# Optimization experiments

Measured on AMD Instinct MI355X. Metric: run time of the kernel, lower is better.

Reference implementation:

```python
import jax, jax.numpy as jnp
import numpy as np
import math

N_EMBD = 1024
N_HEAD = 16
B, T = 2, 2048


def new_gelu(x):
    # GPT-2 tanh-approx GELU (matches torch module exactly)
    return 0.5 * x * (1.0 + jnp.tanh(jnp.sqrt(2.0 / jnp.pi) * (x + 0.044715 * x ** 3)))


def layer_norm(x, w, b, eps=1e-5):
    mu = jnp.mean(x, axis=-1, keepdims=True)
    var = jnp.var(x, axis=-1, keepdims=True)
    return (x - mu) * jax.lax.rsqrt(var + eps) * w + b


def setup_inputs() -> dict:
    key = jax.random.key(0)
    ks = jax.random.split(key, 8)
    C = N_EMBD
    s = 0.02
    return {
        "x": jax.random.normal(ks[0], (B, T, C), dtype=jnp.float32),
        "ln1_w": jnp.ones((C,), jnp.float32),
        "ln1_b": jnp.zeros((C,), jnp.float32),
        "attn_w": s * jax.random.normal(ks[1], (C, 3 * C), jnp.float32),
        "attn_b": jnp.zeros((3 * C,), jnp.float32),
        "attn_proj_w": s * jax.random.normal(ks[2], (C, C), jnp.float32),
        "attn_proj_b": jnp.zeros((C,), jnp.float32),
        "ln2_w": jnp.ones((C,), jnp.float32),
        "ln2_b": jnp.zeros((C,), jnp.float32),
        "fc_w": s * jax.random.normal(ks[3], (C, 4 * C), jnp.float32),
        "fc_b": jnp.zeros((4 * C,), jnp.float32),
        "mlp_proj_w": s * jax.random.normal(ks[4], (4 * C, C), jnp.float32),
        "mlp_proj_b": jnp.zeros((C,), jnp.float32),
    }


def block_forward(x, ln1_w, ln1_b, attn_w, attn_b, attn_proj_w, attn_proj_b,
                  ln2_w, ln2_b, fc_w, fc_b, mlp_proj_w, mlp_proj_b):
    Bm, Tm, C = x.shape
    H = N_HEAD
    D = C // H
    # --- self attention (pre-LN) ---
    h = layer_norm(x, ln1_w, ln1_b)
    qkv = h @ attn_w + attn_b  # [B,T,3C]
    q, k, v = jnp.split(qkv, 3, axis=-1)
    q = q.reshape(Bm, Tm, H, D).transpose(0, 2, 1, 3)  # [B,H,T,D]
    k = k.reshape(Bm, Tm, H, D).transpose(0, 2, 1, 3)
    v = v.reshape(Bm, Tm, H, D).transpose(0, 2, 1, 3)
    att = jnp.einsum('bhqd,bhkd->bhqk', q, k) * (1.0 / math.sqrt(D))
    att = jax.nn.softmax(att, axis=-1)  # NOTE: no causal mask in source
    y = jnp.einsum('bhqk,bhkd->bhqd', att, v)
    y = y.transpose(0, 2, 1, 3).reshape(Bm, Tm, C)
    x = x + (y @ attn_proj_w + attn_proj_b)
    # --- MLP ---
    h = layer_norm(x, ln2_w, ln2_b)
    h = new_gelu(h @ fc_w + fc_b)
    x = x + (h @ mlp_proj_w + mlp_proj_b)
    return x


def reference(x, ln1_w, ln1_b, attn_w, attn_b, attn_proj_w, attn_proj_b,
              ln2_w, ln2_b, fc_w, fc_b, mlp_proj_w, mlp_proj_b):
    return block_forward(x, ln1_w, ln1_b, attn_w, attn_b, attn_proj_w, attn_proj_b,
                         ln2_w, ln2_b, fc_w, fc_b, mlp_proj_w, mlp_proj_b)
```

## Files before the change

kernel.cpp:

```cpp
#include <hip/hip_runtime.h>

typedef __attribute__((ext_vector_type(4)))  float  f32x4;
typedef __attribute__((ext_vector_type(16))) float  f32x16;
typedef __attribute__((ext_vector_type(8)))  short  s16x8;
typedef __attribute__((ext_vector_type(4)))  short  s16x4;
typedef __attribute__((ext_vector_type(4)))  unsigned u32x4;
typedef __attribute__((ext_vector_type(2)))  unsigned u32x2;
typedef __attribute__((ext_vector_type(2)))  int    i32x2;

__device__ __forceinline__ short f2bf(float f) {
    unsigned u = __builtin_bit_cast(unsigned, f);
    u += 0x7fff + ((u >> 16) & 1);
    return (short)(u >> 16);
}

__device__ __forceinline__ void load_lds16(const void* g, void* l) {
    __builtin_amdgcn_global_load_lds(
        (const __attribute__((address_space(1))) unsigned int*)g,
        (__attribute__((address_space(3))) unsigned int*)l, 16, 0, 0);
}

__global__ __launch_bounds__(256) void transpose_cast(const float* __restrict__ W,
                                                      short* __restrict__ Wt,
                                                      int K, int N) {
    __shared__ float t[32][33];
    int n0 = blockIdx.x * 32, k0 = blockIdx.y * 32;
    int tx = threadIdx.x & 31, ty = threadIdx.x >> 5;
#pragma unroll
    for (int i = 0; i < 4; i++)
        t[ty + 8 * i][tx] = W[(size_t)(k0 + ty + 8 * i) * N + n0 + tx];
    __syncthreads();
#pragma unroll
    for (int i = 0; i < 4; i++)
        Wt[(size_t)(n0 + ty + 8 * i) * K + k0 + tx] = f2bf(t[tx][ty + 8 * i]);
}

__global__ __launch_bounds__(256) void vtrans_kernel(const short* __restrict__ qkv,
                                                     short* __restrict__ Vtg) {
    const int T = 2048, C3 = 3072;
    __shared__ short tl[32][33];
    int bh = blockIdx.y >> 1;
    int b = bh >> 4, h = bh & 15;
    int dh = (blockIdx.y & 1) * 32;
    int t0 = blockIdx.x * 32;
    int tx = threadIdx.x & 31, ty = threadIdx.x >> 5;
    const short* src = qkv + (size_t)b * T * C3 + 2048 + h * 64 + dh;
#pragma unroll
    for (int i = 0; i < 4; i++)
        tl[ty + 8 * i][tx] = src[(size_t)(t0 + ty + 8 * i) * C3 + tx];
    __syncthreads();
#pragma unroll
    for (int i = 0; i < 4; i++)
        Vtg[((size_t)bh * 64 + dh + ty + 8 * i) * T + t0 + tx] = tl[tx][ty + 8 * i];
}

__global__ __launch_bounds__(256) void ln_kernel(const float* __restrict__ x,
                                                 const float* __restrict__ w,
                                                 const float* __restrict__ b,
                                                 short* __restrict__ out) {
    int row = blockIdx.x;
    int tid = threadIdx.x;
    const float4 v = ((const float4*)(x + (size_t)row * 1024))[tid];
    float s  = v.x + v.y + v.z + v.w;
    float ss = v.x * v.x + v.y * v.y + v.z * v.z + v.w * v.w;
#pragma unroll
    for (int o = 32; o > 0; o >>= 1) {
        s  += __shfl_down(s, o);
        ss += __shfl_down(ss, o);
    }
    __shared__ float rs[4], rq[4];
    int wave = tid >> 6, lane = tid & 63;
    if (lane == 0) { rs[wave] = s; rq[wave] = ss; }
    __syncthreads();
    float tot = rs[0] + rs[1] + rs[2] + rs[3];
    float tq  = rq[0] + rq[1] + rq[2] + rq[3];
    float mu   = tot * (1.f / 1024.f);
    float var  = tq * (1.f / 1024.f) - mu * mu;
    float rstd = rsqrtf(var + 1e-5f);
    const float4 wv = ((const float4*)w)[tid];
    const float4 bv = ((const float4*)b)[tid];
    s16x4 o;
    o[0] = f2bf((v.x - mu) * rstd * wv.x + bv.x);
    o[1] = f2bf((v.y - mu) * rstd * wv.y + bv.y);
    o[2] = f2bf((v.z - mu) * rstd * wv.z + bv.z);
    o[3] = f2bf((v.w - mu) * rstd * wv.w + bv.w);
    ((s16x4*)(out + (size_t)row * 1024))[tid] = o;
}

template <typename OUT_T, bool GELU, bool RES, bool SCALE_Q>
__global__ __launch_bounds__(256) void gemm_bt(const short* __restrict__ A,
                                               const short* __restrict__ Bt,
                                               const float* __restrict__ bias,
                                               const float* __restrict__ res,
                                               OUT_T* __restrict__ C,
                                               int M, int N, int K) {
    __shared__ __align__(16) short As[128 * 32];
    __shared__ __align__(16) short Bs[128 * 32];
    int tid = threadIdx.x;
    int m0 = blockIdx.y * 128, n0 = blockIdx.x * 128;
    int wave = tid >> 6, lane = tid & 63;
    int wr = wave >> 1, wc = wave & 1;
    int g = lane >> 4, q = lane & 15;
    f32x4 acc[4][4] = {};
    const short* Ab = A + (size_t)m0 * K;
    const short* Bb = Bt + (size_t)n0 * K;
    int srow = tid >> 2;
    int scol = (tid & 3) * 8;
    for (int k0 = 0; k0 < K; k0 += 32) {
        __syncthreads();
        load_lds16(Ab + (size_t)srow * K + k0 + scol, As + tid * 8);
        load_lds16(Ab + (size_t)(srow + 64) * K + k0 + scol, As + 2048 + tid * 8);
        load_lds16(Bb + (size_t)srow * K + k0 + scol, Bs + tid * 8);
        load_lds16(Bb + (size_t)(srow + 64) * K + k0 + scol, Bs + 2048 + tid * 8);
        __syncthreads();
        s16x8 a[4], bf[4];
#pragma unroll
        for (int mi = 0; mi < 4; mi++)
            a[mi] = *(const s16x8*)(As + (wr * 64 + mi * 16 + q) * 32 + g * 8);
#pragma unroll
        for (int ni = 0; ni < 4; ni++)
            bf[ni] = *(const s16x8*)(Bs + (wc * 64 + ni * 16 + q) * 32 + g * 8);
#pragma unroll
        for (int mi = 0; mi < 4; mi++)
#pragma unroll
            for (int ni = 0; ni < 4; ni++)
                acc[mi][ni] = __builtin_amdgcn_mfma_f32_16x16x32_bf16(a[mi], bf[ni], acc[mi][ni], 0, 0, 0);
    }
#pragma unroll
    for (int mi = 0; mi < 4; mi++) {
#pragma unroll
        for (int ni = 0; ni < 4; ni++) {
            int row = m0 + wr * 64 + mi * 16 + g * 4;
            int col = n0 + wc * 64 + ni * 16 + q;
            float bb = bias[col];
#pragma unroll
            for (int r = 0; r < 4; r++) {
                float v = acc[mi][ni][r] + bb;
                if (RES) v += res[(size_t)(row + r) * N + col];
                if (GELU) {
                    float aa = 0.7978845608028654f * (v + 0.044715f * v * v * v);
                    float th = 1.f - 2.f / (__expf(2.f * aa) + 1.f);
                    v = 0.5f * v * (1.f + th);
                }
                if (SCALE_Q && col < 1024) v *= 0.18033688011112042f;
                if constexpr (sizeof(OUT_T) == 2)
                    C[(size_t)(row + r) * N + col] = f2bf(v);
                else
                    C[(size_t)(row + r) * N + col] = v;
            }
        }
    }
}

__global__ __launch_bounds__(256) void gemm_bt_sk(const short* __restrict__ A,
                                                  const short* __restrict__ Bt,
                                                  float* __restrict__ part,
                                                  int M, int N, int K, int Klen) {
    __shared__ __align__(16) short As[128 * 32];
    __shared__ __align__(16) short Bs[128 * 32];
    int tid = threadIdx.x;
    int m0 = blockIdx.y * 128, n0 = blockIdx.x * 128;
    int kz = blockIdx.z;
    int wave = tid >> 6, lane = tid & 63;
    int wr = wave >> 1, wc = wave & 1;
    int g = lane >> 4, q = lane & 15;
    f32x4 acc[4][4] = {};
    const short* Ab = A + (size_t)m0 * K;
    const short* Bb = Bt + (size_t)n0 * K;
    int srow = tid >> 2;
    int scol = (tid & 3) * 8;
    int kend = kz * Klen + Klen;
    for (int k0 = kz * Klen; k0 < kend; k0 += 32) {
        __syncthreads();
        load_lds16(Ab + (size_t)srow * K + k0 + scol, As + tid * 8);
        load_lds16(Ab + (size_t)(srow + 64) * K + k0 + scol, As + 2048 + tid * 8);
        load_lds16(Bb + (size_t)srow * K + k0 + scol, Bs + tid * 8);
        load_lds16(Bb + (size_t)(srow + 64) * K + k0 + scol, Bs + 2048 + tid * 8);
        __syncthreads();
        s16x8 a[4], bf[4];
#pragma unroll
        for (int mi = 0; mi < 4; mi++)
            a[mi] = *(const s16x8*)(As + (wr * 64 + mi * 16 + q) * 32 + g * 8);
#pragma unroll
        for (int ni = 0; ni < 4; ni++)
            bf[ni] = *(const s16x8*)(Bs + (wc * 64 + ni * 16 + q) * 32 + g * 8);
#pragma unroll
        for (int mi = 0; mi < 4; mi++)
#pragma unroll
            for (int ni = 0; ni < 4; ni++)
                acc[mi][ni] = __builtin_amdgcn_mfma_f32_16x16x32_bf16(a[mi], bf[ni], acc[mi][ni], 0, 0, 0);
    }
    float* pb = part + (size_t)kz * M * N;
#pragma unroll
    for (int mi = 0; mi < 4; mi++) {
#pragma unroll
        for (int ni = 0; ni < 4; ni++) {
            int row = m0 + wr * 64 + mi * 16 + g * 4;
            int col = n0 + wc * 64 + ni * 16 + q;
#pragma unroll
            for (int r = 0; r < 4; r++)
                pb[(size_t)(row + r) * N + col] = acc[mi][ni][r];
        }
    }
}

template <int SK>
__global__ __launch_bounds__(256) void reduce_sk(const float* __restrict__ part,
                                                 const float* __restrict__ bias,
                                                 const float* __restrict__ res,
                                                 float* __restrict__ out,
                                                 int MN, int N) {
    int tot = MN >> 2;
    int nb4 = (N >> 2) - 1;
    for (int i = blockIdx.x * 256 + threadIdx.x; i < tot; i += gridDim.x * 256) {
        float4 s = ((const float4*)part)[i];
#pragma unroll
        for (int k = 1; k < SK; k++) {
            float4 p = ((const float4*)(part + (size_t)k * MN))[i];
            s.x += p.x; s.y += p.y; s.z += p.z; s.w += p.w;
        }
        float4 bv = ((const float4*)bias)[i & nb4];
        float4 rv = ((const float4*)res)[i];
        float4 o;
        o.x = s.x + bv.x + rv.x;
        o.y = s.y + bv.y + rv.y;
        o.z = s.z + bv.z + rv.z;
        o.w = s.w + bv.w + rv.w;
        ((float4*)out)[i] = o;
    }
}

__global__ __launch_bounds__(256) void attn_kernel(const short* __restrict__ qkv,
                                                   const short* __restrict__ Vtg,
                                                   short* __restrict__ y) {
    const int T = 2048, C3 = 3072;
    int wg = blockIdx.x;
    int mapped = (wg & 7) * 64 + (wg >> 3);
    int bh = mapped >> 4, qt = mapped & 15;
    int b = bh >> 4, h = bh & 15;
    int tid = threadIdx.x, lane = tid & 63, wave = tid >> 6;
    int ql = lane & 31, hi = lane >> 5;
    const short* base = qkv + (size_t)b * T * C3;

    int qrow = qt * 128 + wave * 32 + ql;
    const short* qp = base + (size_t)qrow * C3 + h * 64;
    s16x8 qf[4];
#pragma unroll
    for (int s = 0; s < 4; s++)
        qf[s] = *(const s16x8*)(qp + ((2 * s + hi) << 3));

    __shared__ __align__(16) short Ks[2][64 * 64];
    __shared__ __align__(16) short Vs[2][64 * 64];

    int srow = tid >> 3, sc8 = tid & 7;
    const short* ksrc = base + 1024 + h * 64 + (size_t)srow * C3 + ((sc8 ^ (srow & 7)) << 3);
    const short* vsrc = Vtg + ((size_t)bh * 64 + srow) * T + ((sc8 ^ (srow & 7)) << 3);

    auto stage = [&](int bi, int t) {
        const short* kp = ksrc + (size_t)(t * 64) * C3;
        load_lds16(kp, &Ks[bi][tid * 8]);
        load_lds16(kp + (size_t)32 * C3, &Ks[bi][tid * 8 + 2048]);
        const short* vp = vsrc + t * 64;
        load_lds16(vp, &Vs[bi][tid * 8]);
        load_lds16(vp + (size_t)32 * T, &Vs[bi][tid * 8 + 2048]);
    };

    float mst = -INFINITY, lst = 0.f;
    f32x16 accY0 = {}, accY1 = {};
    int swz = ql & 7;

    stage(0, 0);
    for (int t = 0; t < 32; ++t) {
        int cur = t & 1;
        __syncthreads();
        if (t < 31) stage(cur ^ 1, t + 1);
        f32x16 s0 = {}, s1 = {};
        const short* kb0 = &Ks[cur][ql * 64];
        const short* kb1 = &Ks[cur][(32 + ql) * 64];
        __builtin_amdgcn_s_setprio(1);
#pragma unroll
        for (int s = 0; s < 4; s++) {
            int c = ((2 * s + hi) ^ swz) << 3;
            s16x8 k0 = *(const s16x8*)(kb0 + c);
            s16x8 k1 = *(const s16x8*)(kb1 + c);
            s0 = __builtin_amdgcn_mfma_f32_32x32x16_bf16(k0, qf[s], s0, 0, 0, 0);
            s1 = __builtin_amdgcn_mfma_f32_32x32x16_bf16(k1, qf[s], s1, 0, 0, 0);
        }
        __builtin_amdgcn_s_setprio(0);
        float tm = fmaxf(s0[0], s0[1]);
#pragma unroll
        for (int r = 2; r < 16; r++) tm = fmaxf(tm, s0[r]);
#pragma unroll
        for (int r = 0; r < 16; r++) tm = fmaxf(tm, s1[r]);
        tm = fmaxf(tm, __shfl_xor(tm, 32));
        if (!__all(tm <= mst + 8.f)) {
            float mnew = fmaxf(mst, tm);
            float alpha = exp2f(mst - mnew);
            lst *= alpha;
#pragma unroll
            for (int r = 0; r < 16; r++) { accY0[r] *= alpha; accY1[r] *= alpha; }
            mst = mnew;
        }
        float ps = 0.f;
#pragma unroll
        for (int r = 0; r < 16; r++) { s0[r] = exp2f(s0[r] - mst); ps += s0[r]; }
#pragma unroll
        for (int r = 0; r < 16; r++) { s1[r] = exp2f(s1[r] - mst); ps += s1[r]; }
        ps += __shfl_xor(ps, 32);
        lst += ps;
        s16x8 pb[4];
#pragma unroll
        for (int s = 0; s < 4; s++) {
            int tt = (s & 1) * 8;
            unsigned lo0, lo1, hi0, hi1;
            if (s < 2) {
                asm("v_cvt_pk_bf16_f32 %0, %1, %2" : "=v"(lo0) : "v"(s0[tt + 0]), "v"(s0[tt + 1]));
                asm("v_cvt_pk_bf16_f32 %0, %1, %2" : "=v"(lo1) : "v"(s0[tt + 2]), "v"(s0[tt + 3]));
                asm("v_cvt_pk_bf16_f32 %0, %1, %2" : "=v"(hi0) : "v"(s0[tt + 4]), "v"(s0[tt + 5]));
                asm("v_cvt_pk_bf16_f32 %0, %1, %2" : "=v"(hi1) : "v"(s0[tt + 6]), "v"(s0[tt + 7]));
            } else {
                asm("v_cvt_pk_bf16_f32 %0, %1, %2" : "=v"(lo0) : "v"(s1[tt + 0]), "v"(s1[tt + 1]));
                asm("v_cvt_pk_bf16_f32 %0, %1, %2" : "=v"(lo1) : "v"(s1[tt + 2]), "v"(s1[tt + 3]));
                asm("v_cvt_pk_bf16_f32 %0, %1, %2" : "=v"(hi0) : "v"(s1[tt + 4]), "v"(s1[tt + 5]));
                asm("v_cvt_pk_bf16_f32 %0, %1, %2" : "=v"(hi1) : "v"(s1[tt + 6]), "v"(s1[tt + 7]));
            }
            i32x2 r0 = __builtin_amdgcn_permlane32_swap((int)hi0, (int)lo0, false, false);
            i32x2 r1 = __builtin_amdgcn_permlane32_swap((int)hi1, (int)lo1, false, false);
            u32x4 w;
            w[0] = (unsigned)r0[1]; w[1] = (unsigned)r1[1];
            w[2] = (unsigned)r0[0]; w[3] = (unsigned)r1[0];
            pb[s] = __builtin_bit_cast(s16x8, w);
        }
        const short* vb0 = &Vs[cur][ql * 64];
        const short* vb1 = &Vs[cur][(32 + ql) * 64];
        __builtin_amdgcn_s_setprio(1);
#pragma unroll
        for (int s = 0; s < 4; s++) {
            int c = ((2 * s + hi) ^ swz) << 3;
            s16x8 v0 = *(const s16x8*)(vb0 + c);
            s16x8 v1 = *(const s16x8*)(vb1 + c);
            accY0 = __builtin_amdgcn_mfma_f32_32x32x16_bf16(v0, pb[s], accY0, 0, 0, 0);
            accY1 = __builtin_amdgcn_mfma_f32_32x32x16_bf16(v1, pb[s], accY1, 0, 0, 0);
        }
        __builtin_amdgcn_s_setprio(0);
    }
    float linv = 1.f / lst;
    short* yrow = y + ((size_t)b * T + qrow) * 1024 + h * 64;
#pragma unroll
    for (int r = 0; r < 4; r++) {
        unsigned w0, w1, w2, w3;
        float a0 = accY0[4 * r] * linv, a1 = accY0[4 * r + 1] * linv;
        float a2 = accY0[4 * r + 2] * linv, a3 = accY0[4 * r + 3] * linv;
        float b0 = accY1[4 * r] * linv, b1 = accY1[4 * r + 1] * linv;
        float b2 = accY1[4 * r + 2] * linv, b3 = accY1[4 * r + 3] * linv;
        asm("v_cvt_pk_bf16_f32 %0, %1, %2" : "=v"(w0) : "v"(a0), "v"(a1));
        asm("v_cvt_pk_bf16_f32 %0, %1, %2" : "=v"(w1) : "v"(a2), "v"(a3));
        asm("v_cvt_pk_bf16_f32 %0, %1, %2" : "=v"(w2) : "v"(b0), "v"(b1));
        asm("v_cvt_pk_bf16_f32 %0, %1, %2" : "=v"(w3) : "v"(b2), "v"(b3));
        u32x2 p0; p0[0] = w0; p0[1] = w1;
        u32x2 p1; p1[0] = w2; p1[1] = w3;
        *(u32x2*)(yrow + 8 * r + 4 * hi)      = p0;
        *(u32x2*)(yrow + 32 + 8 * r + 4 * hi) = p1;
    }
}

extern "C" void kernel_launch(void* const* d_in, const int* in_sizes, int n_in,
                              void* d_out, int out_size, void* d_ws, size_t ws_size,
                              hipStream_t stream) {
    const float* x           = (const float*)d_in[0];
    const float* ln1_w       = (const float*)d_in[1];
    const float* ln1_b       = (const float*)d_in[2];
    const float* attn_w      = (const float*)d_in[3];
    const float* attn_b      = (const float*)d_in[4];
    const float* attn_proj_w = (const float*)d_in[5];
    const float* attn_proj_b = (const float*)d_in[6];
    const float* ln2_w       = (const float*)d_in[7];
    const float* ln2_b       = (const float*)d_in[8];
    const float* fc_w        = (const float*)d_in[9];
    const float* fc_b        = (const float*)d_in[10];
    const float* mlp_proj_w  = (const float*)d_in[11];
    const float* mlp_proj_b  = (const float*)d_in[12];

    const int M = 4096;

    size_t off = 0;
    char* wsb = (char*)d_ws;
    auto alloc = [&](size_t bytes) {
        void* p = wsb + off;
        off += (bytes + 255) & ~(size_t)255;
        return p;
    };
    short* wt_attn  = (short*)alloc(3072ull * 1024 * 2);
    short* wt_proj  = (short*)alloc(1024ull * 1024 * 2);
    short* wt_fc    = (short*)alloc(4096ull * 1024 * 2);
    short* wt_mproj = (short*)alloc(1024ull * 4096 * 2);
    short* h1       = (short*)alloc((size_t)M * 1024 * 2);
    short* qkvb     = (short*)alloc((size_t)M * 3072 * 2);
    short* yb       = (short*)alloc((size_t)M * 1024 * 2);
    float* x1       = (float*)alloc((size_t)M * 1024 * 4);
    short* vtg      = (short*)alloc((size_t)M * 1024 * 2);
    short* h2       = qkvb;

    size_t base_off = off;
    int SK = 0;
    if (ws_size >= base_off + 4ull * M * 1024 * 4) SK = 4;
    else if (ws_size >= base_off + 2ull * M * 1024 * 4) SK = 2;
    float* part = (float*)(wsb + base_off);

    transpose_cast<<<dim3(3072 / 32, 1024 / 32), 256, 0, stream>>>(attn_w, wt_attn, 1024, 3072);
    transpose_cast<<<dim3(1024 / 32, 1024 / 32), 256, 0, stream>>>(attn_proj_w, wt_proj, 1024, 1024);
    transpose_cast<<<dim3(4096 / 32, 1024 / 32), 256, 0, stream>>>(fc_w, wt_fc, 1024, 4096);
    transpose_cast<<<dim3(1024 / 32, 4096 / 32), 256, 0, stream>>>(mlp_proj_w, wt_mproj, 4096, 1024);

    ln_kernel<<<M, 256, 0, stream>>>(x, ln1_w, ln1_b, h1);
    gemm_bt<short, false, false, true><<<dim3(3072 / 128, M / 128), 256, 0, stream>>>(
        h1, wt_attn, attn_b, nullptr, qkvb, M, 3072, 1024);
    vtrans_kernel<<<dim3(2048 / 32, 64), 256, 0, stream>>>(qkvb, vtg);
    attn_kernel<<<512, 256, 0, stream>>>(qkvb, vtg, yb);
    gemm_bt<float, false, true, false><<<dim3(1024 / 128, M / 128), 256, 0, stream>>>(
        yb, wt_proj, attn_proj_b, x, x1, M, 1024, 1024);
    ln_kernel<<<M, 256, 0, stream>>>(x1, ln2_w, ln2_b, h1);
    gemm_bt<short, true, false, false><<<dim3(4096 / 128, M / 128), 256, 0, stream>>>(
        h1, wt_fc, fc_b, nullptr, h2, M, 4096, 1024);

    if (SK == 4) {
        gemm_bt_sk<<<dim3(1024 / 128, M / 128, 4), 256, 0, stream>>>(
            h2, wt_mproj, part, M, 1024, 4096, 1024);
        reduce_sk<4><<<2048, 256, 0, stream>>>(part, mlp_proj_b, x1, (float*)d_out, M * 1024, 1024);
    } else if (SK == 2) {
        gemm_bt_sk<<<dim3(1024 / 128, M / 128, 2), 256, 0, stream>>>(
            h2, wt_mproj, part, M, 1024, 4096, 2048);
        reduce_sk<2><<<2048, 256, 0, stream>>>(part, mlp_proj_b, x1, (float*)d_out, M * 1024, 1024);
    } else {
        gemm_bt<float, false, true, false><<<dim3(1024 / 128, M / 128), 256, 0, stream>>>(
            h2, wt_mproj, mlp_proj_b, x1, (float*)d_out, M, 1024, 4096);
    }
}
```

Before: 308.4 us.

## Split attention over KV halves with a separate merge kernel

When the workspace is large enough, the attention kernel is launched with twice as many workgroups. Each handles half of the key/value sequence and writes fp32 partial outputs plus its running max and sum. A new merge kernel combines the two halves with log-sum-exp weights and writes the bf16 output. The aim is to raise occupancy across CUs, since 512 workgroups is few for the MI355X's CU count, at the cost of extra fp32 partial traffic and one more kernel launch. The row max and sum reductions are also rewritten as tree reductions to shorten dependency chains.

```diff
diff --git a/kernel.cpp b/kernel.cpp
--- a/kernel.cpp
+++ b/kernel.cpp
@@ -18,6 +18,28 @@
     __builtin_amdgcn_global_load_lds(
         (const __attribute__((address_space(1))) unsigned int*)g,
         (__attribute__((address_space(3))) unsigned int*)l, 16, 0, 0);
+}
+
+__device__ __forceinline__ float tmax32(const f32x16& a, const f32x16& b) {
+    float u[16];
+#pragma unroll
+    for (int i = 0; i < 16; i++) u[i] = fmaxf(a[i], b[i]);
+#pragma unroll
+    for (int i = 0; i < 8; i++) u[i] = fmaxf(u[i], u[i + 8]);
+#pragma unroll
+    for (int i = 0; i < 4; i++) u[i] = fmaxf(u[i], u[i + 4]);
+    return fmaxf(fmaxf(u[0], u[2]), fmaxf(u[1], u[3]));
+}
+
+__device__ __forceinline__ float tsum32(const f32x16& a, const f32x16& b) {
+    float u[16];
+#pragma unroll
+    for (int i = 0; i < 16; i++) u[i] = a[i] + b[i];
+#pragma unroll
+    for (int i = 0; i < 8; i++) u[i] += u[i + 8];
+#pragma unroll
+    for (int i = 0; i < 4; i++) u[i] += u[i + 4];
+    return (u[0] + u[2]) + (u[1] + u[3]);
 }
 
 __global__ __launch_bounds__(256) void transpose_cast(const float* __restrict__ W,
@@ -230,13 +252,22 @@
     }
 }
 
+template <int NS>
 __global__ __launch_bounds__(256) void attn_kernel(const short* __restrict__ qkv,
                                                    const short* __restrict__ Vtg,
-                                                   short* __restrict__ y) {
-    const int T = 2048, C3 = 3072;
+                                                   short* __restrict__ y,
+                                                   float* __restrict__ partY,
+                                                   float* __restrict__ ml) {
+    const int T = 2048, C3 = 3072, M = 4096;
     int wg = blockIdx.x;
-    int mapped = (wg & 7) * 64 + (wg >> 3);
-    int bh = mapped >> 4, qt = mapped & 15;
+    int bh, qt, half;
+    if (NS == 1) {
+        int mapped = (wg & 7) * 64 + (wg >> 3);
+        bh = mapped >> 4; qt = mapped & 15; half = 0;
+    } else {
+        int mapped = (wg & 7) * 128 + (wg >> 3);
+        bh = mapped >> 5; qt = (mapped >> 1) & 15; half = mapped & 1;
+    }
     int b = bh >> 4, h = bh & 15;
     int tid = threadIdx.x, lane = tid & 63, wave = tid >> 6;
     int ql = lane & 31, hi = lane >> 5;
@@ -268,12 +299,14 @@
     float mst = -INFINITY, lst = 0.f;
     f32x16 accY0 = {}, accY1 = {};
     int swz = ql & 7;
-
-    stage(0, 0);
-    for (int t = 0; t < 32; ++t) {
-        int cur = t & 1;
+    const int NT = 32 / NS;
+    const int t0 = half * NT;
+
+    stage(0, t0);
+    for (int ti = 0; ti < NT; ++ti) {
+        int cur = ti & 1;
         __syncthreads();
-        if (t < 31) stage(cur ^ 1, t + 1);
+        if (ti < NT - 1) stage(cur ^ 1, t0 + ti + 1);
         f32x16 s0 = {}, s1 = {};
         const short* kb0 = &Ks[cur][ql * 64];
         const short* kb1 = &Ks[cur][(32 + ql) * 64];
@@ -287,11 +320,7 @@
             s1 = __builtin_amdgcn_mfma_f32_32x32x16_bf16(k1, qf[s], s1, 0, 0, 0);
         }
         __builtin_amdgcn_s_setprio(0);
-        float tm = fmaxf(s0[0], s0[1]);
-#pragma unroll
-        for (int r = 2; r < 16; r++) tm = fmaxf(tm, s0[r]);
-#pragma unroll
-        for (int r = 0; r < 16; r++) tm = fmaxf(tm, s1[r]);
+        float tm = tmax32(s0, s1);
         tm = fmaxf(tm, __shfl_xor(tm, 32));
         if (!__all(tm <= mst + 8.f)) {
             float mnew = fmaxf(mst, tm);
@@ -301,11 +330,11 @@
             for (int r = 0; r < 16; r++) { accY0[r] *= alpha; accY1[r] *= alpha; }
             mst = mnew;
         }
-        float ps = 0.f;
-#pragma unroll
-        for (int r = 0; r < 16; r++) { s0[r] = exp2f(s0[r] - mst); ps += s0[r]; }
-#pragma unroll
-        for (int r = 0; r < 16; r++) { s1[r] = exp2f(s1[r] - mst); ps += s1[r]; }
+#pragma unroll
+        for (int r = 0; r < 16; r++) s0[r] = exp2f(s0[r] - mst);
+#pragma unroll
+        for (int r = 0; r < 16; r++) s1[r] = exp2f(s1[r] - mst);
+        float ps = tsum32(s0, s1);
         ps += __shfl_xor(ps, 32);
         lst += ps;
         s16x8 pb[4];
@@ -344,24 +373,59 @@
         }
         __builtin_amdgcn_s_setprio(0);
     }
-    float linv = 1.f / lst;
-    short* yrow = y + ((size_t)b * T + qrow) * 1024 + h * 64;
-#pragma unroll
-    for (int r = 0; r < 4; r++) {
-        unsigned w0, w1, w2, w3;
-        float a0 = accY0[4 * r] * linv, a1 = accY0[4 * r + 1] * linv;
-        float a2 = accY0[4 * r + 2] * linv, a3 = accY0[4 * r + 3] * linv;
-        float b0 = accY1[4 * r] * linv, b1 = accY1[4 * r + 1] * linv;
-        float b2 = accY1[4 * r + 2] * linv, b3 = accY1[4 * r + 3] * linv;
-        asm("v_cvt_pk_bf16_f32 %0, %1, %2" : "=v"(w0) : "v"(a0), "v"(a1));
-        asm("v_cvt_pk_bf16_f32 %0, %1, %2" : "=v"(w1) : "v"(a2), "v"(a3));
-        asm("v_cvt_pk_bf16_f32 %0, %1, %2" : "=v"(w2) : "v"(b0), "v"(b1));
-        asm("v_cvt_pk_bf16_f32 %0, %1, %2" : "=v"(w3) : "v"(b2), "v"(b3));
-        u32x2 p0; p0[0] = w0; p0[1] = w1;
-        u32x2 p1; p1[0] = w2; p1[1] = w3;
-        *(u32x2*)(yrow + 8 * r + 4 * hi)      = p0;
-        *(u32x2*)(yrow + 32 + 8 * r + 4 * hi) = p1;
-    }
+    if (NS == 1) {
+        float linv = 1.f / lst;
+        short* yrow = y + ((size_t)b * T + qrow) * 1024 + h * 64;
+#pragma unroll
+        for (int r = 0; r < 4; r++) {
+            unsigned w0, w1, w2, w3;
+            float a0 = accY0[4 * r] * linv, a1 = accY0[4 * r + 1] * linv;
+            float a2 = accY0[4 * r + 2] * linv, a3 = accY0[4 * r + 3] * linv;
+            float b0 = accY1[4 * r] * linv, b1 = accY1[4 * r + 1] * linv;
+            float b2 = accY1[4 * r + 2] * linv, b3 = accY1[4 * r + 3] * linv;
+            asm("v_cvt_pk_bf16_f32 %0, %1, %2" : "=v"(w0) : "v"(a0), "v"(a1));
+            asm("v_cvt_pk_bf16_f32 %0, %1, %2" : "=v"(w1) : "v"(a2), "v"(a3));
+            asm("v_cvt_pk_bf16_f32 %0, %1, %2" : "=v"(w2) : "v"(b0), "v"(b1));
+            asm("v_cvt_pk_bf16_f32 %0, %1, %2" : "=v"(w3) : "v"(b2), "v"(b3));
+            u32x2 p0; p0[0] = w0; p0[1] = w1;
+            u32x2 p1; p1[0] = w2; p1[1] = w3;
+            *(u32x2*)(yrow + 8 * r + 4 * hi)      = p0;
+            *(u32x2*)(yrow + 32 + 8 * r + 4 * hi) = p1;
+        }
+    } else {
+        float* yp = partY + ((size_t)half * M + (size_t)b * T + qrow) * 1024 + h * 64;
+#pragma unroll
+        for (int r = 0; r < 4; r++) {
+            float4 p0 = make_float4(accY0[4 * r], accY0[4 * r + 1], accY0[4 * r + 2], accY0[4 * r + 3]);
+            float4 p1 = make_float4(accY1[4 * r], accY1[4 * r + 1], accY1[4 * r + 2], accY1[4 * r + 3]);
+            *(float4*)(yp + 8 * r + 4 * hi)      = p0;
+            *(float4*)(yp + 32 + 8 * r + 4 * hi) = p1;
+        }
+        if (hi == 0) {
+            float2 v = make_float2(mst, lst);
+            *(float2*)(ml + ((size_t)b * T + qrow) * 4 + 2 * half) = v;
+        }
+    }
+}
+
+__global__ __launch_bounds__(256) void merge_attn(const float* __restrict__ partY,
+                                                  const float* __restrict__ ml,
+                                                  short* __restrict__ y) {
+    const int M = 4096;
+    int i = blockIdx.x * 256 + threadIdx.x;
+    int row = i >> 8;
+    float4 q = ((const float4*)ml)[row];
+    float m = fmaxf(q.x, q.z);
+    float w0 = exp2f(q.x - m), w1 = exp2f(q.z - m);
+    float li = 1.f / (q.y * w0 + q.w * w1);
+    float4 a = ((const float4*)partY)[i];
+    float4 bq = ((const float4*)(partY + (size_t)M * 1024))[i];
+    s16x4 o;
+    o[0] = f2bf((a.x * w0 + bq.x * w1) * li);
+    o[1] = f2bf((a.y * w0 + bq.y * w1) * li);
+    o[2] = f2bf((a.z * w0 + bq.z * w1) * li);
+    o[3] = f2bf((a.w * w0 + bq.w * w1) * li);
+    ((s16x4*)y)[i] = o;
 }
 
 extern "C" void kernel_launch(void* const* d_in, const int* in_sizes, int n_in,
@@ -399,6 +463,7 @@
     short* yb       = (short*)alloc((size_t)M * 1024 * 2);
     float* x1       = (float*)alloc((size_t)M * 1024 * 4);
     short* vtg      = (short*)alloc((size_t)M * 1024 * 2);
+    float* mlbuf    = (float*)alloc((size_t)M * 4 * 4);
     short* h2       = qkvb;
 
     size_t base_off = off;
@@ -406,6 +471,7 @@
     if (ws_size >= base_off + 4ull * M * 1024 * 4) SK = 4;
     else if (ws_size >= base_off + 2ull * M * 1024 * 4) SK = 2;
     float* part = (float*)(wsb + base_off);
+    bool attn_split = ws_size >= base_off + 2ull * M * 1024 * 4;
 
     transpose_cast<<<dim3(3072 / 32, 1024 / 32), 256, 0, stream>>>(attn_w, wt_attn, 1024, 3072);
     transpose_cast<<<dim3(1024 / 32, 1024 / 32), 256, 0, stream>>>(attn_proj_w, wt_proj, 1024, 1024);
@@ -416,7 +482,12 @@
     gemm_bt<short, false, false, true><<<dim3(3072 / 128, M / 128), 256, 0, stream>>>(
         h1, wt_attn, attn_b, nullptr, qkvb, M, 3072, 1024);
     vtrans_kernel<<<dim3(2048 / 32, 64), 256, 0, stream>>>(qkvb, vtg);
-    attn_kernel<<<512, 256, 0, stream>>>(qkvb, vtg, yb);
+    if (attn_split) {
+        attn_kernel<2><<<1024, 256, 0, stream>>>(qkvb, vtg, nullptr, part, mlbuf);
+        merge_attn<<<M * 1024 / 4 / 256, 256, 0, stream>>>(part, mlbuf, yb);
+    } else {
+        attn_kernel<1><<<512, 256, 0, stream>>>(qkvb, vtg, yb, nullptr, nullptr);
+    }
     gemm_bt<float, false, true, false><<<dim3(1024 / 128, M / 128), 256, 0, stream>>>(
         yb, wt_proj, attn_proj_b, x, x1, M, 1024, 1024);
     ln_kernel<<<M, 256, 0, stream>>>(x1, ln2_w, ln2_b, h1);
```

New measurement: 321.1 us. +4.1%, slower.
